# Performance work log

Hardware: AMD Instinct MI355X
Metric: run time of the kernel (lower is better)

The kernel has to match this reference:

```python
import jax, jax.numpy as jnp
import numpy as np

IN_F, OUT_F = 4096, 11008
B, S = 4, 2048

def setup_inputs() -> dict:
    key = jax.random.key(0)
    k1, k2, k3, k4, k5 = jax.random.split(key, 5)
    x = jax.random.normal(k1, (B, S, IN_F), dtype=jnp.float32)
    packed_weights = jax.random.randint(k2, (OUT_F, IN_F // 2), 0, 256, dtype=jnp.int32)
    scales = jax.random.normal(k3, (OUT_F,), dtype=jnp.float32)
    zero_points = jax.random.randint(k4, (OUT_F,), 0, 15, dtype=jnp.int32)
    bias = jax.random.normal(k5, (1, OUT_F), dtype=jnp.float32)
    return {"x": x, "packed_weights": packed_weights, "scales": scales,
            "zero_points": zero_points, "bias": bias}

def _dequantize(packed_weights, scales, zero_points, dtype):
    # unpack: low nibble first, then high nibble (matches torch stack([low, high], dim=2).view)
    low = packed_weights & 15
    high = (packed_weights >> 4) & 15
    unpacked = jnp.stack([low, high], axis=2).reshape(packed_weights.shape[0], -1)  # [out, in]
    return (unpacked.astype(dtype) - zero_points[:, None].astype(dtype)) * scales[:, None].astype(dtype)

def reference(x, packed_weights, scales, zero_points, bias):
    W = _dequantize(packed_weights, scales, zero_points, x.dtype)  # [out, in]
    out = jnp.einsum('bsi,oi->bso', x, W)  # F.linear
    return out + bias
```

## Files before the change

kernel.cpp:

```cpp
#include <hip/hip_runtime.h>
#include <hip/hip_bf16.h>
#include <stdint.h>

#define IN_F   4096
#define OUT_F  11008
#define M_DIM  8192

#define BM 256
#define BN 256
#define BK 64
#define TM (M_DIM / BM)
#define TN (OUT_F / BN)
#define NWG (TM * TN)
#define KT (IN_F / BK)
#define KC (IN_F / 16)
#define HTB (128 * 64)

typedef __attribute__((ext_vector_type(4))) int   int32x4;
typedef __attribute__((ext_vector_type(8))) short short8;
typedef __attribute__((ext_vector_type(4))) float f32x4;

union Pack8 { __bf16 h[8]; uint4 u; };
union PackI { char c[16]; ::int4 v; };

__device__ inline uint4 pack8_f(float4 f0, float4 f1) {
    Pack8 o;
    o.h[0] = (__bf16)f0.x; o.h[1] = (__bf16)f0.y;
    o.h[2] = (__bf16)f0.z; o.h[3] = (__bf16)f0.w;
    o.h[4] = (__bf16)f1.x; o.h[5] = (__bf16)f1.y;
    o.h[6] = (__bf16)f1.z; o.h[7] = (__bf16)f1.w;
    return o.u;
}

__device__ inline uint4 dequant8(int4 v, float s, float zb) {
    Pack8 o;
    int pv[4] = {v.x, v.y, v.z, v.w};
#pragma unroll
    for (int j = 0; j < 4; ++j) {
        o.h[2 * j]     = (__bf16)fmaf((float)(pv[j] & 15), s, zb);
        o.h[2 * j + 1] = (__bf16)fmaf((float)((pv[j] >> 4) & 15), s, zb);
    }
    return o.u;
}

#define GLOAD_LDS16(g, l)                                                     \
    __builtin_amdgcn_global_load_lds(                                         \
        (const __attribute__((address_space(1))) void*)(g),                   \
        (__attribute__((address_space(3))) void*)(l), 16, 0, 0)

#define BAR()   __builtin_amdgcn_s_barrier()
#define SBAR0() __builtin_amdgcn_sched_barrier(0)
#define VMW(n)  asm volatile("s_waitcnt vmcnt(" #n ")" ::: "memory")

__global__ __launch_bounds__(256) void quant_x_kernel(const float* __restrict__ x,
        char* __restrict__ xq, float* __restrict__ srow) {
    const int row = blockIdx.x;
    const int t   = threadIdx.x;
    const float4* xr = (const float4*)(x + (size_t)row * IN_F) + t * 4;
    float4 v[4];
    float am = 0.f;
#pragma unroll
    for (int j = 0; j < 4; ++j) {
        v[j] = xr[j];
        am = fmaxf(am, fmaxf(fmaxf(fabsf(v[j].x), fabsf(v[j].y)),
                             fmaxf(fabsf(v[j].z), fabsf(v[j].w))));
    }
#pragma unroll
    for (int off = 32; off; off >>= 1) am = fmaxf(am, __shfl_xor(am, off, 64));
    __shared__ float wm4[4];
    if ((t & 63) == 0) wm4[t >> 6] = am;
    __syncthreads();
    am = fmaxf(fmaxf(wm4[0], wm4[1]), fmaxf(wm4[2], wm4[3]));
    const float qs = am > 0.f ? 127.f / am : 0.f;
    if (t == 0) srow[row] = am > 0.f ? am * (1.f / 127.f) : 0.f;
    PackI o;
#pragma unroll
    for (int j = 0; j < 4; ++j) {
        const float* f = (const float*)&v[j];
#pragma unroll
        for (int e = 0; e < 4; ++e) {
            float q = rintf(f[e] * qs);
            q = fminf(127.f, fmaxf(-127.f, q));
            o.c[j * 4 + e] = (char)(int)q;
        }
    }
    ((::int4*)(xq + (size_t)row * IN_F))[t] = o.v;
}

__global__ void deqw_i8_kernel(const int* __restrict__ pw, const int* __restrict__ zps,
                               char* __restrict__ wq, int nChunks) {
    int stride = gridDim.x * blockDim.x;
    for (int c = blockIdx.x * blockDim.x + threadIdx.x; c < nChunks; c += stride) {
        int row = c >> 8;
        int cc  = c & 255;
        int zp  = zps[row];
        const ::int4* p = (const ::int4*)(pw + (size_t)row * (IN_F / 2) + cc * 8);
        ::int4 v0 = p[0], v1 = p[1];
        int pv[8] = {v0.x, v0.y, v0.z, v0.w, v1.x, v1.y, v1.z, v1.w};
        PackI o;
#pragma unroll
        for (int j = 0; j < 8; ++j) {
            o.c[2 * j]     = (char)((pv[j] & 15) - zp);
            o.c[2 * j + 1] = (char)(((pv[j] >> 4) & 15) - zp);
        }
        ((::int4*)wq)[c] = o.v;
    }
}

__device__ inline void stA(char* smem, const uint4* gA, int t, int h, int buf, int wo) {
    GLOAD_LDS16(gA + (size_t)h * 64 * KC + (t & (KT - 1)) * 4,
                smem + ((buf * 2 + 0) * 2 + h) * HTB + wo);
}
__device__ inline void stB(char* smem, const uint4* gB, int t, int h, int buf, int wo) {
    GLOAD_LDS16(gB + (size_t)h * 32 * KC + (t & (KT - 1)) * 4,
                smem + ((buf * 2 + 1) * 2 + h) * HTB + wo);
}

template <int QM>
__device__ inline void read_A(const char* smem, int buf, int wm, int lane, int32x4 (&a)[4]) {
    const char* base = smem + ((buf * 2 + 0) * 2 + QM) * HTB;
    const int pp = lane & 15, q = (lane >> 4) * 16;
#pragma unroll
    for (int mi = 0; mi < 4; ++mi) {
        int row = wm * 64 + mi * 16 + pp;
        a[mi] = *(const int32x4*)(base + row * 64 + (q ^ (((row >> 1) & 3) << 4)));
    }
}

template <int QN>
__device__ inline void read_B(const char* smem, int buf, int wn, int lane, int32x4 (&bq)[2]) {
    const char* base = smem + ((buf * 2 + 1) * 2 + QN) * HTB;
    const int pp = lane & 15, q = (lane >> 4) * 16;
#pragma unroll
    for (int nj = 0; nj < 2; ++nj) {
        int row = wn * 32 + nj * 16 + pp;
        bq[nj] = *(const int32x4*)(base + row * 64 + (q ^ (((row >> 1) & 3) << 4)));
    }
}

template <int QM>
__device__ inline void mfma16both(int32x4 (&a)[4], int32x4 (&b0)[2], int32x4 (&b1)[2],
                                  int32x4 (&acc)[2][4][2][2]) {
    __builtin_amdgcn_s_setprio(1);
#pragma unroll
    for (int mi = 0; mi < 4; ++mi) {
#pragma unroll
        for (int nj = 0; nj < 2; ++nj)
            acc[QM][mi][0][nj] = __builtin_amdgcn_mfma_i32_16x16x64_i8(
                a[mi], b0[nj], acc[QM][mi][0][nj], 0, 0, 0);
#pragma unroll
        for (int nj = 0; nj < 2; ++nj)
            acc[QM][mi][1][nj] = __builtin_amdgcn_mfma_i32_16x16x64_i8(
                a[mi], b1[nj], acc[QM][mi][1][nj], 0, 0, 0);
    }
    __builtin_amdgcn_s_setprio(0);
}

__global__ __launch_bounds__(512, 2) void w4a16_gemm_i8(
    const uint4* __restrict__ xq4, const uint4* __restrict__ wq4,
    const float* __restrict__ srow, const float* __restrict__ scales,
    const float* __restrict__ bias, float* __restrict__ out) {

    extern __shared__ __align__(16) char smem[];

    const int tid  = threadIdx.x;
    const int lane = tid & 63;
    const int wid  = tid >> 6;
    const int wm   = wid >> 2;
    const int wn   = wid & 3;

    const int bid = blockIdx.x;
    const int xcd = bid & 7;
    const int p   = bid >> 3;
    int tm, tn;
    if (p < 160) { int c = p >> 4, q = p & 15; tm = xcd * 4 + (q & 3); tn = c * 4 + (q >> 2); }
    else         { int q = p - 160;            tm = xcd * 4 + (q & 3); tn = 40 + (q >> 2); }
    const int bm0 = tm * BM;
    const int bn0 = tn * BN;

    const int l2  = lane >> 2;
    const int csw = (lane & 3) ^ ((lane >> 3) & 3);
    const uint4* gA = xq4 + (size_t)(bm0 + (wid >> 2) * 128 + (wid & 3) * 16 + l2) * KC + csw;
    const uint4* gB = wq4 + (size_t)(bn0 + (wid >> 1) * 64 + (wid & 1) * 16 + l2) * KC + csw;
    const int wo = wid * 1024;

    int32x4 acc[2][4][2][2];
#pragma unroll
    for (int qm = 0; qm < 2; ++qm)
#pragma unroll
        for (int mi = 0; mi < 4; ++mi)
#pragma unroll
            for (int qn = 0; qn < 2; ++qn)
#pragma unroll
                for (int nj = 0; nj < 2; ++nj) acc[qm][mi][qn][nj] = {0, 0, 0, 0};

    int32x4 a[4];
    int32x4 b[2][2];

    stA(smem, gA, 0, 0, 0, wo); stB(smem, gB, 0, 0, 0, wo);
    stB(smem, gB, 0, 1, 0, wo); stA(smem, gA, 0, 1, 0, wo);
    stA(smem, gA, 1, 0, 1, wo); stB(smem, gB, 1, 0, 1, wo);
    stB(smem, gB, 1, 1, 1, wo);
    VMW(3); SBAR0(); BAR();

    for (int i = 0; i < KT / 2; ++i) {
        const int to = 2 * i + 1, t2 = 2 * i + 2, t3 = 2 * i + 3;
        read_A<0>(smem, 0, wm, lane, a);
        read_B<0>(smem, 0, wn, lane, b[0]);
        read_B<1>(smem, 0, wn, lane, b[1]);
        stA(smem, gA, to, 1, 1, wo);
        BAR(); mfma16both<0>(a, b[0], b[1], acc); BAR();
        read_A<1>(smem, 0, wm, lane, a);
        stA(smem, gA, t2, 0, 0, wo);
        stB(smem, gB, t2, 0, 0, wo);
        stB(smem, gB, t2, 1, 0, wo);
        VMW(3); SBAR0(); BAR();
        mfma16both<1>(a, b[0], b[1], acc); BAR();
        read_A<0>(smem, 1, wm, lane, a);
        read_B<0>(smem, 1, wn, lane, b[0]);
        read_B<1>(smem, 1, wn, lane, b[1]);
        stA(smem, gA, t2, 1, 0, wo);
        BAR(); mfma16both<0>(a, b[0], b[1], acc); BAR();
        read_A<1>(smem, 1, wm, lane, a);
        stA(smem, gA, t3, 0, 1, wo);
        stB(smem, gB, t3, 0, 1, wo);
        stB(smem, gB, t3, 1, 1, wo);
        VMW(3); SBAR0(); BAR();
        mfma16both<1>(a, b[0], b[1], acc); BAR();
    }
    VMW(0);

#pragma unroll
    for (int qm = 0; qm < 2; ++qm)
#pragma unroll
        for (int mi = 0; mi < 4; ++mi) {
            int row0 = bm0 + wm * 128 + qm * 64 + mi * 16 + (lane >> 4) * 4;
            float sr[4];
#pragma unroll
            for (int rr = 0; rr < 4; ++rr) sr[rr] = srow[row0 + rr];
#pragma unroll
            for (int qn = 0; qn < 2; ++qn)
#pragma unroll
                for (int nj = 0; nj < 2; ++nj) {
                    int col  = bn0 + wn * 64 + qn * 32 + nj * 16 + (lane & 15);
                    float sc = scales[col];
                    float bv = bias[col];
#pragma unroll
                    for (int rr = 0; rr < 4; ++rr)
                        __builtin_nontemporal_store(
                            (float)acc[qm][mi][qn][nj][rr] * (sr[rr] * sc) + bv,
                            &out[(size_t)(row0 + rr) * OUT_F + col]);
                }
        }
}

#define FBM 128
#define FBN 128
#define FTM (M_DIM / FBM)
#define FTN (OUT_F / FBN)
#define FNWG (FTM * FTN)

__global__ __launch_bounds__(256) void w4a16_gemm_fb(
    const float* __restrict__ xf,
    const int* __restrict__ pw,
    const float* __restrict__ scales, const int* __restrict__ zps,
    const float* __restrict__ bias, float* __restrict__ out) {

    __shared__ __align__(16) __bf16 As[FBM * 64];
    __shared__ __align__(16) __bf16 Bs[FBN * 64];

    const int tid  = threadIdx.x;
    const int lane = tid & 63;
    const int wid  = tid >> 6;
    const int wm   = wid >> 1;
    const int wn   = wid & 1;

    int orig = blockIdx.x;
    int wg   = (orig & 7) * (FNWG / 8) + (orig >> 3);
    const int bm0 = (wg / FTN) * FBM;
    const int bn0 = (wg % FTN) * FBN;

    f32x4 acc[4][4];
#pragma unroll
    for (int i = 0; i < 4; ++i)
#pragma unroll
        for (int j = 0; j < 4; ++j) acc[i][j] = {0.f, 0.f, 0.f, 0.f};

    for (int kt = 0; kt < IN_F / 64; ++kt) {
#pragma unroll
        for (int i = 0; i < 4; ++i) {
            int ci  = i * 256 + tid;
            int row = ci >> 3, c8 = ci & 7;
            const float4* pp = (const float4*)(xf + (size_t)(bm0 + row) * IN_F + kt * 64 + c8 * 8);
            uint4 d = pack8_f(pp[0], pp[1]);
            *(uint4*)((char*)As + row * 128 + ((c8 * 16) ^ ((row & 7) << 4))) = d;
        }
#pragma unroll
        for (int i = 0; i < 4; ++i) {
            int ci  = i * 256 + tid;
            int row = ci >> 3, c8 = ci & 7;
            int r    = bn0 + row;
            float s  = scales[r];
            float zb = -s * (float)zps[r];
            int4 v = *(const int4*)(pw + (size_t)r * (IN_F / 2) + kt * 32 + c8 * 4);
            uint4 d = dequant8(v, s, zb);
            *(uint4*)((char*)Bs + row * 128 + ((c8 * 16) ^ ((row & 7) << 4))) = d;
        }
        __syncthreads();

#pragma unroll
        for (int kk = 0; kk < 2; ++kk) {
            short8 a[4], b[4];
#pragma unroll
            for (int mi = 0; mi < 4; ++mi) {
                int row = wm * 64 + mi * 16 + (lane & 15);
                a[mi] = *(const short8*)((const char*)As + row * 128 +
                                         ((kk * 64 + (lane >> 4) * 16) ^ ((row & 7) << 4)));
            }
#pragma unroll
            for (int ni = 0; ni < 4; ++ni) {
                int row = wn * 64 + ni * 16 + (lane & 15);
                b[ni] = *(const short8*)((const char*)Bs + row * 128 +
                                         ((kk * 64 + (lane >> 4) * 16) ^ ((row & 7) << 4)));
            }
#pragma unroll
            for (int mi = 0; mi < 4; ++mi)
#pragma unroll
                for (int ni = 0; ni < 4; ++ni)
                    acc[mi][ni] = __builtin_amdgcn_mfma_f32_16x16x32_bf16(a[mi], b[ni], acc[mi][ni], 0, 0, 0);
        }
        __syncthreads();
    }

#pragma unroll
    for (int ni = 0; ni < 4; ++ni) {
        int col  = bn0 + wn * 64 + ni * 16 + (lane & 15);
        float bv = bias[col];
#pragma unroll
        for (int mi = 0; mi < 4; ++mi) {
            int row0 = bm0 + wm * 64 + mi * 16 + (lane >> 4) * 4;
#pragma unroll
            for (int r = 0; r < 4; ++r)
                out[(size_t)(row0 + r) * OUT_F + col] = acc[mi][ni][r] + bv;
        }
    }
}

extern "C" void kernel_launch(void* const* d_in, const int* in_sizes, int n_in,
                              void* d_out, int out_size, void* d_ws, size_t ws_size,
                              hipStream_t stream) {
    const float* x      = (const float*)d_in[0];
    const int* pw       = (const int*)d_in[1];
    const float* scales = (const float*)d_in[2];
    const int* zps      = (const int*)d_in[3];
    const float* bias   = (const float*)d_in[4];
    float* out          = (float*)d_out;

    const size_t xq_bytes = (size_t)M_DIM * IN_F;
    const size_t sr_bytes = 65536;
    const size_t wq_bytes = (size_t)OUT_F * IN_F;
    const bool predeq = ws_size >= xq_bytes + sr_bytes + wq_bytes;

    if (predeq) {
        char*  xq   = (char*)d_ws;
        float* srow = (float*)((char*)d_ws + xq_bytes);
        char*  wq   = (char*)d_ws + xq_bytes + sr_bytes;
        quant_x_kernel<<<dim3(M_DIM), dim3(256), 0, stream>>>(x, xq, srow);
        deqw_i8_kernel<<<dim3(2048), dim3(256), 0, stream>>>(pw, zps, wq, OUT_F * (IN_F / 16));
        (void)hipFuncSetAttribute((const void*)w4a16_gemm_i8,
                                  hipFuncAttributeMaxDynamicSharedMemorySize, 65536);
        w4a16_gemm_i8<<<dim3(NWG), dim3(512), 65536, stream>>>(
            (const uint4*)xq, (const uint4*)wq, srow, scales, bias, out);
    } else {
        w4a16_gemm_fb<<<dim3(FNWG), dim3(256), 0, stream>>>(x, pw, scales, zps, bias, out);
    }
}
```

Baseline: 441.3 us.

## Double-buffer LDS fragment registers to overlap LDS reads with MFMA

```diff
diff --git a/kernel.cpp b/kernel.cpp
--- a/kernel.cpp
+++ b/kernel.cpp
@@ -48,9 +48,10 @@
         (const __attribute__((address_space(1))) void*)(g),                   \
         (__attribute__((address_space(3))) void*)(l), 16, 0, 0)
 
-#define BAR()   __builtin_amdgcn_s_barrier()
+#define BAR()   do { __builtin_amdgcn_s_barrier(); __builtin_amdgcn_sched_barrier(0); } while (0)
 #define SBAR0() __builtin_amdgcn_sched_barrier(0)
-#define VMW(n)  asm volatile("s_waitcnt vmcnt(" #n ")" ::: "memory")
+#define VMW(n)  do { asm volatile("s_waitcnt vmcnt(" #n ")" ::: "memory"); __builtin_amdgcn_sched_barrier(0); } while (0)
+#define LGKM(n) do { asm volatile("s_waitcnt lgkmcnt(" #n ")" ::: "memory"); __builtin_amdgcn_sched_barrier(0); } while (0)
 
 __global__ __launch_bounds__(256) void quant_x_kernel(const float* __restrict__ x,
         char* __restrict__ xq, float* __restrict__ srow) {
@@ -194,41 +195,58 @@
 #pragma unroll
                 for (int nj = 0; nj < 2; ++nj) acc[qm][mi][qn][nj] = {0, 0, 0, 0};
 
-    int32x4 a[4];
-    int32x4 b[2][2];
+    int32x4 aA[4], aB[4];
+    int32x4 bA[2][2], bB[2][2];
 
     stA(smem, gA, 0, 0, 0, wo); stB(smem, gB, 0, 0, 0, wo);
     stB(smem, gB, 0, 1, 0, wo); stA(smem, gA, 0, 1, 0, wo);
     stA(smem, gA, 1, 0, 1, wo); stB(smem, gB, 1, 0, 1, wo);
     stB(smem, gB, 1, 1, 1, wo);
-    VMW(3); SBAR0(); BAR();
+    VMW(3);
+    BAR();
+    read_A<0>(smem, 0, wm, lane, aA);
+    read_B<0>(smem, 0, wn, lane, bA[0]);
+    read_B<1>(smem, 0, wn, lane, bA[1]);
 
     for (int i = 0; i < KT / 2; ++i) {
         const int to = 2 * i + 1, t2 = 2 * i + 2, t3 = 2 * i + 3;
-        read_A<0>(smem, 0, wm, lane, a);
-        read_B<0>(smem, 0, wn, lane, b[0]);
-        read_B<1>(smem, 0, wn, lane, b[1]);
         stA(smem, gA, to, 1, 1, wo);
-        BAR(); mfma16both<0>(a, b[0], b[1], acc); BAR();
-        read_A<1>(smem, 0, wm, lane, a);
+        BAR();
+        read_A<1>(smem, 0, wm, lane, aB);
+        LGKM(4);
+        mfma16both<0>(aA, bA[0], bA[1], acc);
+        BAR();
         stA(smem, gA, t2, 0, 0, wo);
         stB(smem, gB, t2, 0, 0, wo);
         stB(smem, gB, t2, 1, 0, wo);
-        VMW(3); SBAR0(); BAR();
-        mfma16both<1>(a, b[0], b[1], acc); BAR();
-        read_A<0>(smem, 1, wm, lane, a);
-        read_B<0>(smem, 1, wn, lane, b[0]);
-        read_B<1>(smem, 1, wn, lane, b[1]);
+        VMW(3);
+        BAR();
+        read_A<0>(smem, 1, wm, lane, aA);
+        read_B<0>(smem, 1, wn, lane, bB[0]);
+        read_B<1>(smem, 1, wn, lane, bB[1]);
+        LGKM(8);
+        mfma16both<1>(aB, bA[0], bA[1], acc);
+        BAR();
         stA(smem, gA, t2, 1, 0, wo);
-        BAR(); mfma16both<0>(a, b[0], b[1], acc); BAR();
-        read_A<1>(smem, 1, wm, lane, a);
+        BAR();
+        read_A<1>(smem, 1, wm, lane, aB);
+        LGKM(4);
+        mfma16both<0>(aA, bB[0], bB[1], acc);
+        BAR();
         stA(smem, gA, t3, 0, 1, wo);
         stB(smem, gB, t3, 0, 1, wo);
         stB(smem, gB, t3, 1, 1, wo);
-        VMW(3); SBAR0(); BAR();
-        mfma16both<1>(a, b[0], b[1], acc); BAR();
+        VMW(3);
+        BAR();
+        read_A<0>(smem, 0, wm, lane, aA);
+        read_B<0>(smem, 0, wn, lane, bA[0]);
+        read_B<1>(smem, 0, wn, lane, bA[1]);
+        LGKM(8);
+        mfma16both<1>(aB, bB[0], bB[1], acc);
+        BAR();
     }
     VMW(0);
+    LGKM(0);
 
 #pragma unroll
     for (int qm = 0; qm < 2; ++qm)
```

Result: no change. 446.2 us (+1.1%).
